# Performance work log

Hardware: AMD Instinct MI355X
Metric: run time of the kernel (lower is better)

Reference implementation:

```python
import jax, jax.numpy as jnp
import numpy as np

B, N, D = 4, 4096, 64

def setup_inputs() -> dict:
    key = jax.random.key(0)
    inputs = jax.random.normal(key, (B, N, D), dtype=jnp.float32)
    return {"inputs": inputs}

def reference(inputs) -> jnp.ndarray:
    # similarity = X X^T : [B, N, N]
    similarity = jnp.einsum('bnd,bmd->bnm', inputs, inputs)
    # row softmax over last axis -> adjacency
    adjacency = jax.nn.softmax(similarity, axis=-1)
    return adjacency
```

## Files before the change

kernel.cpp:

```cpp
#include <hip/hip_runtime.h>

#define B_ 4
#define N_ 4096
#define D_ 64

typedef __bf16 bf16_t;
typedef bf16_t bf16x8 __attribute__((ext_vector_type(8)));
typedef float f32x16 __attribute__((ext_vector_type(16)));

__global__ void conv_norm_kernel(const float* __restrict__ X,
                                 bf16_t* __restrict__ Xb,
                                 float* __restrict__ norms) {
    int row = blockIdx.x * 4 + (threadIdx.x >> 6);
    int d   = threadIdx.x & 63;
    size_t idx = (size_t)row * D_ + d;
    float x = X[idx];
    Xb[idx] = (bf16_t)x;
    float sq = x * x;
    #pragma unroll
    for (int off = 32; off; off >>= 1) sq += __shfl_xor(sq, off);
    if (d == 0) norms[row] = sq;
}

__device__ __forceinline__ f32x16 tile_mm(const bf16_t* __restrict__ brow,
                                          bf16x8 a0, bf16x8 a1,
                                          bf16x8 a2, bf16x8 a3) {
    bf16x8 b0 = *(const bf16x8*)(brow);
    bf16x8 b1 = *(const bf16x8*)(brow + 16);
    bf16x8 b2 = *(const bf16x8*)(brow + 32);
    bf16x8 b3 = *(const bf16x8*)(brow + 48);
    f32x16 acc;
    #pragma unroll
    for (int i = 0; i < 16; ++i) acc[i] = 0.0f;
    acc = __builtin_amdgcn_mfma_f32_32x32x16_bf16(a0, b0, acc, 0, 0, 0);
    acc = __builtin_amdgcn_mfma_f32_32x32x16_bf16(a1, b1, acc, 0, 0, 0);
    acc = __builtin_amdgcn_mfma_f32_32x32x16_bf16(a2, b2, acc, 0, 0, 0);
    acc = __builtin_amdgcn_mfma_f32_32x32x16_bf16(a3, b3, acc, 0, 0, 0);
    return acc;
}

__global__ __launch_bounds__(256) void softmax_xxt_kernel(
        const bf16_t* __restrict__ Xb,
        const float* __restrict__ norms,
        float* __restrict__ Out) {
    const int tid  = threadIdx.x;
    const int wave = tid >> 6;
    const int lane = tid & 63;
    const int b    = blockIdx.x >> 7;
    const int rowbase = (blockIdx.x & 127) * 32;

    const bf16_t* Xbb = Xb + (size_t)b * N_ * D_;
    const int mcol = lane & 31;
    const int half = lane >> 5;

    const bf16_t* arow = Xbb + (size_t)(rowbase + mcol) * D_ + half * 8;
    const bf16x8 a0 = *(const bf16x8*)(arow);
    const bf16x8 a1 = *(const bf16x8*)(arow + 16);
    const bf16x8 a2 = *(const bf16x8*)(arow + 32);
    const bf16x8 a3 = *(const bf16x8*)(arow + 48);

    float lse[16];
    {
        const float* nb = norms + b * N_ + rowbase;
        #pragma unroll
        for (int r = 0; r < 16; ++r) {
            int row = (r & 3) + 8 * (r >> 2) + 4 * half;
            lse[r] = nb[row];
        }
    }

    __shared__ float partials[4][32];

    float sums[16];
    #pragma unroll
    for (int r = 0; r < 16; ++r) sums[r] = 0.0f;

    for (int t = 0; t < N_ / 128; ++t) {
        const int c0 = t * 128 + wave * 32;
        const bf16_t* brow = Xbb + (size_t)(c0 + mcol) * D_ + half * 8;
        f32x16 acc = tile_mm(brow, a0, a1, a2, a3);
        #pragma unroll
        for (int r = 0; r < 16; ++r) sums[r] += __expf(acc[r] - lse[r]);
    }

    #pragma unroll
    for (int r = 0; r < 16; ++r) {
        float s = sums[r];
        s += __shfl_xor(s, 1);
        s += __shfl_xor(s, 2);
        s += __shfl_xor(s, 4);
        s += __shfl_xor(s, 8);
        s += __shfl_xor(s, 16);
        sums[r] = s;
    }

    if (mcol == 0) {
        #pragma unroll
        for (int r = 0; r < 16; ++r) {
            int row = (r & 3) + 8 * (r >> 2) + 4 * half;
            partials[wave][row] = sums[r];
        }
    }
    __syncthreads();

    #pragma unroll
    for (int r = 0; r < 16; ++r) {
        int row = (r & 3) + 8 * (r >> 2) + 4 * half;
        float tot = partials[0][row] + partials[1][row] +
                    partials[2][row] + partials[3][row];
        lse[r] += __logf(tot);
    }

    float* outb = Out + (size_t)b * N_ * N_;
    for (int t = 0; t < N_ / 128; ++t) {
        const int c0 = t * 128 + wave * 32;
        const bf16_t* brow = Xbb + (size_t)(c0 + mcol) * D_ + half * 8;
        f32x16 acc = tile_mm(brow, a0, a1, a2, a3);
        #pragma unroll
        for (int r = 0; r < 16; ++r) {
            int row = rowbase + (r & 3) + 8 * (r >> 2) + 4 * half;
            outb[(size_t)row * N_ + (c0 + mcol)] = __expf(acc[r] - lse[r]);
        }
    }
}

extern "C" void kernel_launch(void* const* d_in, const int* in_sizes, int n_in,
                              void* d_out, int out_size, void* d_ws, size_t ws_size,
                              hipStream_t stream) {
    const float* X = (const float*)d_in[0];
    float* Out     = (float*)d_out;

    bf16_t* Xb   = (bf16_t*)d_ws;
    float*  norms = (float*)((char*)d_ws + (size_t)B_ * N_ * D_ * sizeof(bf16_t));

    conv_norm_kernel<<<(B_ * N_) / 4, 256, 0, stream>>>(X, Xb, norms);
    softmax_xxt_kernel<<<(B_ * N_) / 32, 256, 0, stream>>>(Xb, norms, Out);
}
```

Baseline: 305.8 us.

## Pre-swizzle bf16 operand into MFMA fragment order and use nontemporal output stores

The conversion kernel now writes X in bf16 in a layout that matches the MFMA operand fragments, so each lane's 16-byte loads in the GEMM tiles are contiguous across the wavefront instead of strided by row. Norms are computed with a shared-memory reduction in the same kernel. The 256 MB output is written with nontemporal stores so it does not pollute the caches. The main cost is still the output write bandwidth, so the layout change may matter little.

```diff
diff --git a/kernel.cpp b/kernel.cpp
--- a/kernel.cpp
+++ b/kernel.cpp
@@ -3,32 +3,57 @@
 #define B_ 4
 #define N_ 4096
 #define D_ 64
+#define NG (N_ / 32)
 
 typedef __bf16 bf16_t;
 typedef bf16_t bf16x8 __attribute__((ext_vector_type(8)));
 typedef float f32x16 __attribute__((ext_vector_type(16)));
+typedef float f32x4 __attribute__((ext_vector_type(4)));
 
-__global__ void conv_norm_kernel(const float* __restrict__ X,
-                                 bf16_t* __restrict__ Xb,
-                                 float* __restrict__ norms) {
-    int row = blockIdx.x * 4 + (threadIdx.x >> 6);
-    int d   = threadIdx.x & 63;
-    size_t idx = (size_t)row * D_ + d;
-    float x = X[idx];
-    Xb[idx] = (bf16_t)x;
-    float sq = x * x;
+__global__ __launch_bounds__(256) void swizzle_norm_kernel(
+        const float* __restrict__ X,
+        bf16_t* __restrict__ Bs,
+        float* __restrict__ norms) {
+    const int tid  = threadIdx.x;
+    const int kb   = tid >> 6;
+    const int lane = tid & 63;
+    const int mcol = lane & 31;
+    const int half = lane >> 5;
+    const int b = blockIdx.x >> 7;
+    const int g = blockIdx.x & (NG - 1);
+
+    const int row = g * 32 + mcol;
+    const float* src = X + (size_t)(b * N_ + row) * D_ + kb * 16 + half * 8;
+    f32x4 x0 = *(const f32x4*)(src);
+    f32x4 x1 = *(const f32x4*)(src + 4);
+
+    bf16x8 v;
+    float p = 0.f;
     #pragma unroll
-    for (int off = 32; off; off >>= 1) sq += __shfl_xor(sq, off);
-    if (d == 0) norms[row] = sq;
+    for (int j = 0; j < 4; ++j) { v[j]     = (bf16_t)x0[j]; p += x0[j] * x0[j]; }
+    #pragma unroll
+    for (int j = 0; j < 4; ++j) { v[4 + j] = (bf16_t)x1[j]; p += x1[j] * x1[j]; }
+
+    bf16_t* dst = Bs + ((size_t)((b * NG + g) * 4 + kb)) * 512 + lane * 8;
+    *(bf16x8*)dst = v;
+
+    p += __shfl_xor(p, 32);
+    __shared__ float pn[4][32];
+    if (half == 0) pn[kb][mcol] = p;
+    __syncthreads();
+    if (tid < 32)
+        norms[b * N_ + g * 32 + tid] =
+            pn[0][tid] + pn[1][tid] + pn[2][tid] + pn[3][tid];
 }
 
-__device__ __forceinline__ f32x16 tile_mm(const bf16_t* __restrict__ brow,
+__device__ __forceinline__ f32x16 tile_mm(const bf16_t* __restrict__ chunk,
+                                          int lane,
                                           bf16x8 a0, bf16x8 a1,
                                           bf16x8 a2, bf16x8 a3) {
-    bf16x8 b0 = *(const bf16x8*)(brow);
-    bf16x8 b1 = *(const bf16x8*)(brow + 16);
-    bf16x8 b2 = *(const bf16x8*)(brow + 32);
-    bf16x8 b3 = *(const bf16x8*)(brow + 48);
+    bf16x8 b0 = *(const bf16x8*)(chunk + lane * 8);
+    bf16x8 b1 = *(const bf16x8*)(chunk + 512 + lane * 8);
+    bf16x8 b2 = *(const bf16x8*)(chunk + 1024 + lane * 8);
+    bf16x8 b3 = *(const bf16x8*)(chunk + 1536 + lane * 8);
     f32x16 acc;
     #pragma unroll
     for (int i = 0; i < 16; ++i) acc[i] = 0.0f;
@@ -40,24 +65,24 @@
 }
 
 __global__ __launch_bounds__(256) void softmax_xxt_kernel(
-        const bf16_t* __restrict__ Xb,
+        const bf16_t* __restrict__ Bs,
         const float* __restrict__ norms,
         float* __restrict__ Out) {
     const int tid  = threadIdx.x;
     const int wave = tid >> 6;
     const int lane = tid & 63;
     const int b    = blockIdx.x >> 7;
-    const int rowbase = (blockIdx.x & 127) * 32;
-
-    const bf16_t* Xbb = Xb + (size_t)b * N_ * D_;
-    const int mcol = lane & 31;
+    const int ga   = blockIdx.x & (NG - 1);
+    const int rowbase = ga * 32;
     const int half = lane >> 5;
 
-    const bf16_t* arow = Xbb + (size_t)(rowbase + mcol) * D_ + half * 8;
-    const bf16x8 a0 = *(const bf16x8*)(arow);
-    const bf16x8 a1 = *(const bf16x8*)(arow + 16);
-    const bf16x8 a2 = *(const bf16x8*)(arow + 32);
-    const bf16x8 a3 = *(const bf16x8*)(arow + 48);
+    const bf16_t* Bsb = Bs + (size_t)(b * NG) * 2048;
+
+    const bf16_t* achunk = Bsb + (size_t)ga * 2048;
+    const bf16x8 a0 = *(const bf16x8*)(achunk + lane * 8);
+    const bf16x8 a1 = *(const bf16x8*)(achunk + 512 + lane * 8);
+    const bf16x8 a2 = *(const bf16x8*)(achunk + 1024 + lane * 8);
+    const bf16x8 a3 = *(const bf16x8*)(achunk + 1536 + lane * 8);
 
     float lse[16];
     {
@@ -75,10 +100,9 @@
     #pragma unroll
     for (int r = 0; r < 16; ++r) sums[r] = 0.0f;
 
-    for (int t = 0; t < N_ / 128; ++t) {
-        const int c0 = t * 128 + wave * 32;
-        const bf16_t* brow = Xbb + (size_t)(c0 + mcol) * D_ + half * 8;
-        f32x16 acc = tile_mm(brow, a0, a1, a2, a3);
+    for (int t = 0; t < NG / 4; ++t) {
+        const int g = t * 4 + wave;
+        f32x16 acc = tile_mm(Bsb + (size_t)g * 2048, lane, a0, a1, a2, a3);
         #pragma unroll
         for (int r = 0; r < 16; ++r) sums[r] += __expf(acc[r] - lse[r]);
     }
@@ -94,6 +118,7 @@
         sums[r] = s;
     }
 
+    const int mcol = lane & 31;
     if (mcol == 0) {
         #pragma unroll
         for (int r = 0; r < 16; ++r) {
@@ -112,14 +137,15 @@
     }
 
     float* outb = Out + (size_t)b * N_ * N_;
-    for (int t = 0; t < N_ / 128; ++t) {
-        const int c0 = t * 128 + wave * 32;
-        const bf16_t* brow = Xbb + (size_t)(c0 + mcol) * D_ + half * 8;
-        f32x16 acc = tile_mm(brow, a0, a1, a2, a3);
+    for (int t = 0; t < NG / 4; ++t) {
+        const int g = t * 4 + wave;
+        const int c0 = g * 32;
+        f32x16 acc = tile_mm(Bsb + (size_t)g * 2048, lane, a0, a1, a2, a3);
         #pragma unroll
         for (int r = 0; r < 16; ++r) {
             int row = rowbase + (r & 3) + 8 * (r >> 2) + 4 * half;
-            outb[(size_t)row * N_ + (c0 + mcol)] = __expf(acc[r] - lse[r]);
+            float v = __expf(acc[r] - lse[r]);
+            __builtin_nontemporal_store(v, &outb[(size_t)row * N_ + (c0 + mcol)]);
         }
     }
 }
@@ -130,9 +156,9 @@
     const float* X = (const float*)d_in[0];
     float* Out     = (float*)d_out;
 
-    bf16_t* Xb   = (bf16_t*)d_ws;
+    bf16_t* Bs    = (bf16_t*)d_ws;
     float*  norms = (float*)((char*)d_ws + (size_t)B_ * N_ * D_ * sizeof(bf16_t));
 
-    conv_norm_kernel<<<(B_ * N_) / 4, 256, 0, stream>>>(X, Xb, norms);
-    softmax_xxt_kernel<<<(B_ * N_) / 32, 256, 0, stream>>>(Xb, norms, Out);
+    swizzle_norm_kernel<<<B_ * NG, 256, 0, stream>>>(X, Bs, norms);
+    softmax_xxt_kernel<<<B_ * NG, 256, 0, stream>>>(Bs, norms, Out);
 }
```

Measured after the change: 309.7 us. No clear change (+1.3%).
